# Kernel tuning notes

Hardware: AMD Instinct MI355X
Metric: run time of the kernel (lower is better)

Reference implementation:

```python
import jax, jax.numpy as jnp
import numpy as np

N, E, C, K = 50000, 800000, 64, 8
D = C * K  # 512
NEG_SLOPE = 0.01  # torch leaky_relu default


def setup_inputs() -> dict:
    key = jax.random.key(0)
    ks = jax.random.split(key, 6)
    x = jax.random.normal(ks[0], (N, D), dtype=jnp.float32)
    edge_index = jax.random.randint(ks[1], (2, E), 0, N, dtype=jnp.int64)
    conv_W = jax.random.normal(ks[2], (K, C, C), dtype=jnp.float32) * (1.0 / np.sqrt(C))
    conv_b = jax.random.normal(ks[3], (K, C), dtype=jnp.float32) * 0.01
    W1 = jax.random.normal(ks[4], (D, D), dtype=jnp.float32) * (1.0 / np.sqrt(D))
    W2 = jax.random.normal(ks[5], (D, D), dtype=jnp.float32) * (1.0 / np.sqrt(D))
    return {"x": x, "edge_index": edge_index, "conv_W": conv_W,
            "conv_b": conv_b, "W1": W1, "W2": W2}


def _gcn_conv(xk, Wk, bk, src, dst, dinv, n):
    # PyG GCNConv: transform, then symmetric-normalized aggregation with self-loops,
    # then add bias.
    xt = xk @ Wk.T  # [N, C]
    norm = dinv[src] * dinv[dst]  # [E]
    agg = jax.ops.segment_sum(norm[:, None] * xt[src], dst, num_segments=n)
    agg = agg + (dinv * dinv)[:, None] * xt  # self-loop contribution
    return agg + bk


def reference(x, edge_index, conv_W, conv_b, W1, W2):
    n = x.shape[0]
    src, dst = edge_index[0], edge_index[1]
    # degree with self-loops (edge weight 1)
    deg = jax.ops.segment_sum(jnp.ones((E,), x.dtype), dst, num_segments=n) + 1.0
    dinv = deg ** -0.5
    xr = x.reshape(n, C, K)
    zs = [jax.nn.leaky_relu(_gcn_conv(xr[:, :, i], conv_W[i], conv_b[i], src, dst, dinv, n),
                            negative_slope=NEG_SLOPE)
          for i in range(K)]
    z = jnp.concatenate(zs, axis=1)  # [N, D]
    z = jax.nn.leaky_relu(z, negative_slope=NEG_SLOPE)
    # dropout is identity in eval mode (dr=12 is invalid for torch Dropout anyway)
    z_fc1 = z @ W1.T
    z_fc2 = z @ W2.T
    s = jnp.sum(z_fc1.T @ z_fc2, axis=0)  # [D]
    # softmax over axis 0 of a [1, D] tensor (as in the original code)
    gate = jax.nn.softmax((s / jnp.sqrt(jnp.asarray(D, x.dtype)))[None, :], axis=0)
    return z * gate
```

## Files before the change

kernel.cpp:

```cpp
#include <hip/hip_runtime.h>

#define NN 50000
#define EE 800000
#define KK 8
#define DD 512
#define CAP 64

typedef __attribute__((ext_vector_type(8))) short short8;
typedef __attribute__((ext_vector_type(4))) float f32x4;
typedef __attribute__((ext_vector_type(4))) unsigned u32x4;

__device__ __forceinline__ float leaky2(float v) {
    v = (v < 0.0f) ? 0.01f * v : v;
    v = (v < 0.0f) ? 0.01f * v : v;
    return v;
}

__device__ __forceinline__ unsigned short f2bf(float f) {
    unsigned u = __float_as_uint(f);
    u += 0x7fffu + ((u >> 16) & 1u);
    return (unsigned short)(u >> 16);
}
__device__ __forceinline__ float bf_lo(unsigned u) { return __uint_as_float(u << 16); }
__device__ __forceinline__ float bf_hi(unsigned u) { return __uint_as_float(u & 0xffff0000u); }

__device__ __forceinline__ void add8(float acc[8], u32x4 v) {
    acc[0] += bf_lo(v[0]); acc[1] += bf_hi(v[0]);
    acc[2] += bf_lo(v[1]); acc[3] += bf_hi(v[1]);
    acc[4] += bf_lo(v[2]); acc[5] += bf_hi(v[2]);
    acc[6] += bf_lo(v[3]); acc[7] += bf_hi(v[3]);
}

__global__ void k_zero(int* __restrict__ cursor) {
    int i = blockIdx.x * 256 + threadIdx.x;
    if (i < NN) cursor[i] = 0;
}

__global__ void k_wconv(const float* __restrict__ W, unsigned short* __restrict__ Wbf) {
    int i = blockIdx.x * 256 + threadIdx.x;
    if (i < KK * 64 * 64) Wbf[i] = f2bf(W[i]);
}

__global__ void k_fill(const int* __restrict__ ei, int* __restrict__ cursor,
                       int* __restrict__ bw) {
    int e0 = (blockIdx.x * 256 + threadIdx.x) * 4;
    if (e0 < EE) {
        int4 s4 = *(const int4*)&ei[e0];
        int4 d4 = *(const int4*)&ei[EE + e0];
        int p;
        p = atomicAdd(&cursor[d4.x], 1); if (p < CAP) bw[(size_t)d4.x * CAP + p] = s4.x;
        p = atomicAdd(&cursor[d4.y], 1); if (p < CAP) bw[(size_t)d4.y * CAP + p] = s4.y;
        p = atomicAdd(&cursor[d4.z], 1); if (p < CAP) bw[(size_t)d4.z * CAP + p] = s4.z;
        p = atomicAdd(&cursor[d4.w], 1); if (p < CAP) bw[(size_t)d4.w * CAP + p] = s4.w;
    }
}

__global__ void k_dinv(const int* __restrict__ cursor, float* __restrict__ dinv) {
    int i = blockIdx.x * 256 + threadIdx.x;
    if (i < NN) dinv[i] = rsqrtf((float)cursor[i] + 1.0f);
}

__global__ __launch_bounds__(256) void k_transform(const float* __restrict__ x,
                                                   const unsigned short* __restrict__ Wbf,
                                                   const float* __restrict__ dinv,
                                                   unsigned short* __restrict__ xt) {
    __shared__ unsigned short lxT[32 * 8 * 64];
    const int t = threadIdx.x;
    const int n0 = blockIdx.x * 32;

    const float4* x4 = (const float4*)x;
    #pragma unroll
    for (int i = 0; i < 16; i++) {
        int idx = i * 256 + t;
        int n = idx >> 7;
        int q = idx & 127;
        int n_eff = n0 + n; if (n_eff >= NN) n_eff = NN - 1;
        float4 v = x4[(size_t)n_eff * 128 + q];
        int c = q >> 1;
        int k0 = (q & 1) * 4;
        unsigned short* p = &lxT[(n * 8 + k0) * 64 + c];
        p[0] = f2bf(v.x); p[64] = f2bf(v.y); p[128] = f2bf(v.z); p[192] = f2bf(v.w);
    }
    __syncthreads();

    const int wv   = t >> 6;
    const int lane = t & 63;
    const int l15  = lane & 15;
    const int quad = lane >> 4;
    const f32x4 zero = {0.f, 0.f, 0.f, 0.f};

    #pragma unroll
    for (int kk = 0; kk < 2; kk++) {
        const int k = wv * 2 + kk;
        short8 afr[4][2];
        #pragma unroll
        for (int jt = 0; jt < 4; jt++)
            #pragma unroll
            for (int ks = 0; ks < 2; ks++)
                afr[jt][ks] = *(const short8*)&Wbf[k * 4096 + (jt * 16 + l15) * 64 + ks * 32 + quad * 8];

        #pragma unroll
        for (int ng = 0; ng < 2; ng++) {
            short8 bfr[2];
            #pragma unroll
            for (int ks = 0; ks < 2; ks++)
                bfr[ks] = *(const short8*)&lxT[((ng * 16 + l15) * 8 + k) * 64 + ks * 32 + quad * 8];
            f32x4 acc[4];
            #pragma unroll
            for (int jt = 0; jt < 4; jt++) {
                acc[jt] = zero;
                acc[jt] = __builtin_amdgcn_mfma_f32_16x16x32_bf16(afr[jt][0], bfr[0], acc[jt], 0, 0, 0);
                acc[jt] = __builtin_amdgcn_mfma_f32_16x16x32_bf16(afr[jt][1], bfr[1], acc[jt], 0, 0, 0);
            }
            const int node = n0 + ng * 16 + l15;
            if (node < NN) {
                const float dv = dinv[node];
                #pragma unroll
                for (int jt = 0; jt < 4; jt++) {
                    ushort4 h;
                    h.x = f2bf(acc[jt][0] * dv); h.y = f2bf(acc[jt][1] * dv);
                    h.z = f2bf(acc[jt][2] * dv); h.w = f2bf(acc[jt][3] * dv);
                    *(ushort4*)&xt[(size_t)node * DD + k * 64 + jt * 16 + quad * 4] = h;
                }
            }
        }
    }
}

__global__ __launch_bounds__(256) void k_agg(const unsigned short* __restrict__ xt,
                                             const float* __restrict__ dinv,
                                             const int* __restrict__ cursor,
                                             const int* __restrict__ bw,
                                             const float* __restrict__ bias,
                                             float* __restrict__ out) {
    const int n = __builtin_amdgcn_readfirstlane(blockIdx.x * 4 + (threadIdx.x >> 6));
    const int lane = threadIdx.x & 63;
    const float dn = dinv[n];
    int cn = cursor[n]; if (cn > CAP) cn = CAP;

    const u32x4* xt4 = (const u32x4*)xt;
    int bidx = bw[(size_t)n * CAP + lane];
    u32x4 a = xt4[(size_t)n * 64 + lane];

    float acc[8];
    acc[0] = bf_lo(a[0]); acc[1] = bf_hi(a[0]);
    acc[2] = bf_lo(a[1]); acc[3] = bf_hi(a[1]);
    acc[4] = bf_lo(a[2]); acc[5] = bf_hi(a[2]);
    acc[6] = bf_lo(a[3]); acc[7] = bf_hi(a[3]);

    int i = 0;
    for (; i + 3 < cn; i += 4) {
        int s0 = __builtin_amdgcn_readlane(bidx, i);
        int s1 = __builtin_amdgcn_readlane(bidx, i + 1);
        int s2 = __builtin_amdgcn_readlane(bidx, i + 2);
        int s3 = __builtin_amdgcn_readlane(bidx, i + 3);
        u32x4 v0 = xt4[((size_t)s0 << 6) + lane];
        u32x4 v1 = xt4[((size_t)s1 << 6) + lane];
        u32x4 v2 = xt4[((size_t)s2 << 6) + lane];
        u32x4 v3 = xt4[((size_t)s3 << 6) + lane];
        __builtin_amdgcn_sched_barrier(0);
        add8(acc, v0); add8(acc, v1); add8(acc, v2); add8(acc, v3);
    }
    if (i + 1 < cn) {
        int s0 = __builtin_amdgcn_readlane(bidx, i);
        int s1 = __builtin_amdgcn_readlane(bidx, i + 1);
        u32x4 v0 = xt4[((size_t)s0 << 6) + lane];
        u32x4 v1 = xt4[((size_t)s1 << 6) + lane];
        add8(acc, v0); add8(acc, v1);
        i += 2;
    }
    if (i < cn) {
        int s0 = __builtin_amdgcn_readlane(bidx, i);
        u32x4 v0 = xt4[((size_t)s0 << 6) + lane];
        add8(acc, v0);
    }

    const float4* b4 = (const float4*)bias;
    float4 b0 = b4[lane * 2], b1 = b4[lane * 2 + 1];
    f32x4 r0, r1;
    r0[0] = leaky2(dn * acc[0] + b0.x); r0[1] = leaky2(dn * acc[1] + b0.y);
    r0[2] = leaky2(dn * acc[2] + b0.z); r0[3] = leaky2(dn * acc[3] + b0.w);
    r1[0] = leaky2(dn * acc[4] + b1.x); r1[1] = leaky2(dn * acc[5] + b1.y);
    r1[2] = leaky2(dn * acc[6] + b1.z); r1[3] = leaky2(dn * acc[7] + b1.w);
    f32x4* o4 = (f32x4*)(out + (size_t)n * DD);
    __builtin_nontemporal_store(r0, o4 + lane * 2);
    __builtin_nontemporal_store(r1, o4 + lane * 2 + 1);
}

extern "C" void kernel_launch(void* const* d_in, const int* in_sizes, int n_in,
                              void* d_out, int out_size, void* d_ws, size_t ws_size,
                              hipStream_t stream) {
    const float* x  = (const float*)d_in[0];
    const int*   ei = (const int*)d_in[1];
    const float* W  = (const float*)d_in[2];
    const float* b  = (const float*)d_in[3];
    float* out = (float*)d_out;

    unsigned short* xt = (unsigned short*)d_ws;
    float* dinv   = (float*)(xt + (size_t)NN * DD);
    int*   cursor = (int*)(dinv + NN);
    int*   bw     = cursor + NN;
    unsigned short* wbf = (unsigned short*)(bw + (size_t)NN * CAP);

    k_zero <<<(NN + 255) / 256, 256, 0, stream>>>(cursor);
    k_wconv<<<(KK * 64 * 64 + 255) / 256, 256, 0, stream>>>(W, wbf);
    k_fill <<<(EE / 4 + 255) / 256, 256, 0, stream>>>(ei, cursor, bw);
    k_dinv <<<(NN + 255) / 256, 256, 0, stream>>>(cursor, dinv);
    k_transform<<<(NN + 31) / 32, 256, 0, stream>>>(x, wbf, dinv, xt);
    k_agg<<<NN / 4, 256, 0, stream>>>(xt, dinv, cursor, bw, b, out);
}
```

Measured before the change: 377.8 us.

## Stream neighbor rows through an LDS ring via async global_load_lds in aggregation

The gather loop in the aggregation kernel now issues direct global-to-LDS loads into a 4-deep per-wave ring buffer. It waits on vmcnt so that four row fetches stay in flight continuously, replacing the batch-of-four register loads that stalled at each batch boundary. The aim is a steadier stream of memory-level parallelism with less register pressure. In exchange it adds LDS round trips, manual waitcnt handling that depends on exact ordering of the counters, and extra per-wave shared memory.

Result: slower. 385.6 us (+2.1%).

```diff
diff --git a/kernel.cpp b/kernel.cpp
--- a/kernel.cpp
+++ b/kernel.cpp
@@ -10,6 +10,9 @@
 typedef __attribute__((ext_vector_type(4))) float f32x4;
 typedef __attribute__((ext_vector_type(4))) unsigned u32x4;
 
+#define WAITV(N) do { asm volatile("s_waitcnt vmcnt(" #N ")" ::: "memory"); \
+                      __builtin_amdgcn_sched_barrier(0); } while (0)
+
 __device__ __forceinline__ float leaky2(float v) {
     v = (v < 0.0f) ? 0.01f * v : v;
     v = (v < 0.0f) ? 0.01f * v : v;
@@ -29,6 +32,14 @@
     acc[2] += bf_lo(v[1]); acc[3] += bf_hi(v[1]);
     acc[4] += bf_lo(v[2]); acc[5] += bf_hi(v[2]);
     acc[6] += bf_lo(v[3]); acc[7] += bf_hi(v[3]);
+}
+
+__device__ __forceinline__ void fetch_row(const unsigned short* xt, int s, int lane,
+                                          unsigned char* lslot) {
+    const unsigned char* g = (const unsigned char*)(xt + ((size_t)s << 9)) + lane * 16;
+    __builtin_amdgcn_global_load_lds((const __attribute__((address_space(1))) void*)g,
+                                     (__attribute__((address_space(3))) void*)lslot,
+                                     16, 0, 0);
 }
 
 __global__ void k_zero(int* __restrict__ cursor) {
@@ -133,47 +144,59 @@
                                              const int* __restrict__ bw,
                                              const float* __restrict__ bias,
                                              float* __restrict__ out) {
-    const int n = __builtin_amdgcn_readfirstlane(blockIdx.x * 4 + (threadIdx.x >> 6));
+    __shared__ __attribute__((aligned(16))) unsigned char ring[4][4][1024];
+    const int wv   = threadIdx.x >> 6;
+    const int n    = __builtin_amdgcn_readfirstlane(blockIdx.x * 4 + wv);
     const int lane = threadIdx.x & 63;
     const float dn = dinv[n];
     int cn = cursor[n]; if (cn > CAP) cn = CAP;
 
     const u32x4* xt4 = (const u32x4*)xt;
     int bidx = bw[(size_t)n * CAP + lane];
-    u32x4 a = xt4[(size_t)n * 64 + lane];
+    u32x4 a = xt4[((size_t)n << 6) + lane];
 
     float acc[8];
     acc[0] = bf_lo(a[0]); acc[1] = bf_hi(a[0]);
     acc[2] = bf_lo(a[1]); acc[3] = bf_hi(a[1]);
     acc[4] = bf_lo(a[2]); acc[5] = bf_hi(a[2]);
     acc[6] = bf_lo(a[3]); acc[7] = bf_hi(a[3]);
-
-    int i = 0;
-    for (; i + 3 < cn; i += 4) {
-        int s0 = __builtin_amdgcn_readlane(bidx, i);
-        int s1 = __builtin_amdgcn_readlane(bidx, i + 1);
-        int s2 = __builtin_amdgcn_readlane(bidx, i + 2);
-        int s3 = __builtin_amdgcn_readlane(bidx, i + 3);
-        u32x4 v0 = xt4[((size_t)s0 << 6) + lane];
-        u32x4 v1 = xt4[((size_t)s1 << 6) + lane];
-        u32x4 v2 = xt4[((size_t)s2 << 6) + lane];
-        u32x4 v3 = xt4[((size_t)s3 << 6) + lane];
+    asm volatile("" :: "v"(dn));
+    __builtin_amdgcn_sched_barrier(0);
+
+    if (cn > 0) fetch_row(xt, __builtin_amdgcn_readlane(bidx, 0), lane, &ring[wv][0][0]);
+    if (cn > 1) fetch_row(xt, __builtin_amdgcn_readlane(bidx, 1), lane, &ring[wv][1][0]);
+    if (cn > 2) fetch_row(xt, __builtin_amdgcn_readlane(bidx, 2), lane, &ring[wv][2][0]);
+    if (cn > 3) fetch_row(xt, __builtin_amdgcn_readlane(bidx, 3), lane, &ring[wv][3][0]);
+
+    for (int i = 0; i < cn - 4; ++i) {
+        WAITV(3);
+        u32x4 v = *(const u32x4*)&ring[wv][i & 3][lane * 16];
+        asm volatile("s_waitcnt lgkmcnt(0)" ::: "memory");
         __builtin_amdgcn_sched_barrier(0);
-        add8(acc, v0); add8(acc, v1); add8(acc, v2); add8(acc, v3);
-    }
-    if (i + 1 < cn) {
-        int s0 = __builtin_amdgcn_readlane(bidx, i);
-        int s1 = __builtin_amdgcn_readlane(bidx, i + 1);
-        u32x4 v0 = xt4[((size_t)s0 << 6) + lane];
-        u32x4 v1 = xt4[((size_t)s1 << 6) + lane];
-        add8(acc, v0); add8(acc, v1);
-        i += 2;
-    }
-    if (i < cn) {
-        int s0 = __builtin_amdgcn_readlane(bidx, i);
-        u32x4 v0 = xt4[((size_t)s0 << 6) + lane];
-        add8(acc, v0);
-    }
+        fetch_row(xt, __builtin_amdgcn_readlane(bidx, i + 4), lane, &ring[wv][i & 3][0]);
+        add8(acc, v);
+    }
+
+    {
+        int base = cn > 4 ? cn - 4 : 0;
+        int rem  = cn - base;
+        if (rem == 4) {
+            WAITV(3); add8(acc, *(const u32x4*)&ring[wv][(base + 0) & 3][lane * 16]);
+            WAITV(2); add8(acc, *(const u32x4*)&ring[wv][(base + 1) & 3][lane * 16]);
+            WAITV(1); add8(acc, *(const u32x4*)&ring[wv][(base + 2) & 3][lane * 16]);
+            WAITV(0); add8(acc, *(const u32x4*)&ring[wv][(base + 3) & 3][lane * 16]);
+        } else if (rem == 3) {
+            WAITV(2); add8(acc, *(const u32x4*)&ring[wv][0][lane * 16]);
+            WAITV(1); add8(acc, *(const u32x4*)&ring[wv][1][lane * 16]);
+            WAITV(0); add8(acc, *(const u32x4*)&ring[wv][2][lane * 16]);
+        } else if (rem == 2) {
+            WAITV(1); add8(acc, *(const u32x4*)&ring[wv][0][lane * 16]);
+            WAITV(0); add8(acc, *(const u32x4*)&ring[wv][1][lane * 16]);
+        } else if (rem == 1) {
+            WAITV(0); add8(acc, *(const u32x4*)&ring[wv][0][lane * 16]);
+        }
+    }
+    __builtin_amdgcn_sched_barrier(0);
 
     const float4* b4 = (const float4*)bias;
     float4 b0 = b4[lane * 2], b1 = b4[lane * 2 + 1];
```
